# Performance work log

Hardware: AMD Instinct MI355X
Metric: run time of the kernel (lower is better)

Reference implementation:

```python
import jax, jax.numpy as jnp
import numpy as np

ACT_SCALE = 1.0 / 12.0  # nn-EUCLID scale
HIDDEN = 32
BATCH = 1048576


def setup_inputs() -> dict:
    key = jax.random.key(0)
    ks = jax.random.split(key, 12)
    H = HIDDEN

    def xavier(k, shape):
        fan_out, fan_in = shape
        std = (2.0 / (fan_in + fan_out)) ** 0.5
        return jax.random.normal(k, shape, jnp.float32) * std

    def bias(k, fan_in, n):
        bound = 1.0 / (fan_in ** 0.5)
        return jax.random.uniform(k, (n,), jnp.float32, -bound, bound)

    return {
        "eps_flat": jax.random.normal(ks[0], (BATCH, 3), jnp.float32) * 0.1,
        "Bf_w": xavier(ks[1], (H, 2)),
        "Bf_b": bias(ks[2], 2, H),
        "A1": jax.random.normal(ks[3], (H, H), jnp.float32) * 0.05,
        "B1_w": xavier(ks[4], (H, 2)),
        "B1_b": bias(ks[5], 2, H),
        "A2": jax.random.normal(ks[6], (H, H), jnp.float32) * 0.05,
        "B2_w": xavier(ks[7], (H, 2)),
        "B2_b": bias(ks[8], 2, H),
        "A_out": jax.random.normal(ks[9], (1, H), jnp.float32) * 0.05,
        "Bo_w": xavier(ks[10], (1, 2)),
        "Bo_b": bias(ks[11], 2, 1),
    }


def reference(eps_flat, Bf_w, Bf_b, A1, B1_w, B1_b, A2, B2_w, B2_b, A_out, Bo_w, Bo_b):
    sp = jax.nn.softplus

    def W_fn(z0):  # z0: (n, 2) -> (n, 1); ICNN potential (dropout p=0 -> identity)
        z = sp(z0 @ Bf_w.T + Bf_b)
        z = ACT_SCALE * sp(z @ sp(A1).T) ** 2 + sp(z0 @ B1_w.T + B1_b)
        z = ACT_SCALE * sp(z @ sp(A2).T) ** 2 + sp(z0 @ B2_w.T + B2_b)
        return z @ sp(A_out).T + z0 @ Bo_w.T + Bo_b

    e11 = eps_flat[:, 0]
    e22 = eps_flat[:, 1]
    e12 = eps_flat[:, 2]
    I1 = e11 + e22
    I2 = e11 ** 2 + 2.0 * e12 ** 2 + e22 ** 2
    z0 = jnp.stack([I1, I2], axis=-1)  # (B, 2)

    # Reference-point gradient at z0_ref = 0 (makes W(0)=0, dW(0)=0 after correction)
    z0_ref = jnp.zeros((1, 2), eps_flat.dtype)
    grad_ref = jax.grad(lambda z: W_fn(z).sum())(z0_ref)  # (1, 2)

    # Per-sample gradient of corrected potential (rows independent -> grad of sum)
    grads = jax.grad(
        lambda z: (W_fn(z) - (z * grad_ref).sum(-1, keepdims=True)).sum()
    )(z0)  # (B, 2)

    dW_dI1 = grads[:, 0]
    dW_dI2 = grads[:, 1]
    sg = jax.lax.stop_gradient
    s11 = dW_dI1 + 2.0 * sg(e11) * dW_dI2
    s22 = dW_dI1 + 2.0 * sg(e22) * dW_dI2
    s12 = 2.0 * sg(e12) * dW_dI2
    return jnp.stack([s11, s22, s12], axis=-1)
```

## Files before the change

### kernel.cpp

```cpp
#include <hip/hip_runtime.h>
#include <hip/hip_fp16.h>
#include <math.h>

#define ACT_SCALE_F (1.0f / 12.0f)
#define LOG2E_F 1.44269504088896340736f
#define LN2_F   0.69314718055994530942f

typedef __attribute__((ext_vector_type(8))) _Float16 half8;
typedef __attribute__((ext_vector_type(4))) float f32x4;
typedef __attribute__((ext_vector_type(4))) unsigned int uint4v;


__device__ __forceinline__ void sp_sig(float x, float& sp, float& sig) {
    float t = __builtin_amdgcn_exp2f(-fabsf(x) * LOG2E_F);
    float u = 1.0f + t;
    float r = __builtin_amdgcn_rcpf(u);
    sp = fmaf(__builtin_amdgcn_logf(u), LN2_F, fmaxf(x, 0.0f));
    sig = (x >= 0.0f) ? r : t * r;
}

__device__ __forceinline__ float sp_only(float x) {
    float t = __builtin_amdgcn_exp2f(-fabsf(x) * LOG2E_F);
    return fmaf(__builtin_amdgcn_logf(1.0f + t), LN2_F, fmaxf(x, 0.0f));
}

__device__ __forceinline__ float sig_only(float x) {
    float t = __builtin_amdgcn_exp2f(-fabsf(x) * LOG2E_F);
    float r = __builtin_amdgcn_rcpf(1.0f + t);
    return (x >= 0.0f) ? r : t * r;
}

__global__ void prep_kernel(const float* __restrict__ Bf_w, const float* __restrict__ Bf_b,
                            const float* __restrict__ A1,
                            const float* __restrict__ B1_w, const float* __restrict__ B1_b,
                            const float* __restrict__ A2,
                            const float* __restrict__ B2_w, const float* __restrict__ B2_b,
                            const float* __restrict__ A_out,
                            float* __restrict__ ws)
{
    __shared__ float sA1[1024], sA2[1024], sAout[32];
    __shared__ float vbufA[32], vbufB[32];
    __shared__ float part0[32], part1[32];
    const int tid = threadIdx.x;

    for (int e = tid; e < 1024; e += 64) {
        sA1[e] = sp_only(A1[e]);
        sA2[e] = sp_only(A2[e]);
    }
    if (tid < 32) {
        float ao = sp_only(A_out[tid]);
        sAout[tid] = ao;
        ws[384 + tid] = ao;
    }
    __syncthreads();

    unsigned int* wsu = (unsigned int*)ws;
    for (int e = tid; e < 512; e += 64) {
        const int mv = e >> 7, u = (e >> 6) & 1, ln = e & 63;
        const int g = ln >> 4, cc = ln & 15, m = 16 * u + cc;
        for (int q = 0; q < 4; ++q) {
            unsigned int word = 0;
            for (int h = 0; h < 2; ++h) {
                const int s8 = 2 * q + h;
                const int k = 16 * (s8 >> 2) + 4 * g + (s8 & 3);
                float v;
                if (mv == 0)      v = sA1[m * 32 + k];
                else if (mv == 1) v = sA2[m * 32 + k];
                else if (mv == 2) v = sA2[k * 32 + m];
                else              v = sA1[k * 32 + m];
                unsigned short hb = __half_as_ushort(__float2half(v));
                word |= ((unsigned int)hb) << (16 * h);
            }
            wsu[512 + 4 * e + q] = word;
        }
    }

    for (int e = tid; e < 512; e += 64) {
        const int l = e >> 3, s8 = e & 7;
        const int g = l >> 4;
        const int k = 16 * (s8 >> 2) + 4 * g + (s8 & 3);
        ws[2560 + 4 * e]     = Bf_w[2 * k];
        ws[2560 + 4 * e + 1] = Bf_w[2 * k + 1];
        ws[2560 + 4 * e + 2] = Bf_b[k];
        ws[2560 + 4 * e + 3] = 0.f;
        ws[4608 + 4 * e]     = B1_w[2 * k];
        ws[4608 + 4 * e + 1] = B1_w[2 * k + 1];
        ws[4608 + 4 * e + 2] = B1_b[k];
        ws[4608 + 4 * e + 3] = 0.f;
        ws[6656 + 4 * e]     = B2_w[2 * k];
        ws[6656 + 4 * e + 1] = B2_w[2 * k + 1];
        ws[6656 + 4 * e + 2] = B2_b[k];
        ws[6656 + 4 * e + 3] = sAout[k];
    }

    const int i = tid;
    float su1 = 0.f, g1 = 0.f, sb1 = 0.f;
    if (tid < 32) {
        float h0;
        sp_sig(Bf_b[i], h0, su1);
        vbufA[i] = h0;
    }
    __syncthreads();
    if (tid < 32) {
        float a1 = 0.f;
        for (int j = 0; j < 32; ++j) a1 = fmaf(vbufA[j], sA1[i * 32 + j], a1);
        float s1, sa1; sp_sig(a1, s1, sa1);
        g1 = 2.0f * ACT_SCALE_F * s1 * sa1;
        float spb1; sp_sig(B1_b[i], spb1, sb1);
        vbufB[i] = fmaf(ACT_SCALE_F * s1, s1, spb1);
    }
    __syncthreads();
    if (tid < 32) {
        float a2 = 0.f;
        for (int j = 0; j < 32; ++j) a2 = fmaf(vbufB[j], sA2[i * 32 + j], a2);
        float s2, sa2; sp_sig(a2, s2, sa2);
        float g2 = 2.0f * ACT_SCALE_F * s2 * sa2;
        float sb2 = sig_only(B2_b[i]);
        float ao = sAout[i];
        part0[i] = ao * sb2 * B2_w[i * 2 + 0];
        part1[i] = ao * sb2 * B2_w[i * 2 + 1];
        vbufA[i] = ao * g2;
    }
    __syncthreads();
    if (tid < 32) {
        float dz1 = 0.f;
        for (int ii = 0; ii < 32; ++ii) dz1 = fmaf(vbufA[ii], sA2[ii * 32 + i], dz1);
        part0[i] += dz1 * sb1 * B1_w[i * 2 + 0];
        part1[i] += dz1 * sb1 * B1_w[i * 2 + 1];
        vbufB[i] = dz1 * g1;
    }
    __syncthreads();
    if (tid < 32) {
        float dh0 = 0.f;
        for (int ii = 0; ii < 32; ++ii) dh0 = fmaf(vbufB[ii], sA1[ii * 32 + i], dh0);
        part0[i] += dh0 * su1 * Bf_w[i * 2 + 0];
        part1[i] += dh0 * su1 * Bf_w[i * 2 + 1];
    }
    __syncthreads();
    if (tid == 0) {
        float r0 = 0.f, r1 = 0.f;
        for (int j = 0; j < 32; ++j) { r0 += part0[j]; r1 += part1[j]; }
        ws[448] = r0;
        ws[449] = r1;
    }
}

#define DSEL(ch, s8) ((ch) == 0 ? ((s8) < 4 ? dA0[(s8) & 3] : dA1[(s8) & 3]) \
                                : ((s8) < 4 ? dB0[(s8) & 3] : dB1[(s8) & 3]))

__global__ void __launch_bounds__(64, 2) icnn_main(
    const float* __restrict__ eps,
    const float* __restrict__ ws,
    float* __restrict__ out, int n)
{
    const int lane = threadIdx.x;
    const int c = lane & 15;

    int idx0 = blockIdx.x * 32 + c;
    int idx1 = idx0 + 16;
    if (idx0 >= n) idx0 = n - 1;
    if (idx1 >= n) idx1 = n - 1;

    const uint4v* __restrict__ ft = (const uint4v*)((const unsigned int*)ws + 512);
    const float4* __restrict__ Qf = (const float4*)(ws + 2560) + lane * 8;
    const float4* __restrict__ Q1 = (const float4*)(ws + 4608) + lane * 8;
    const float4* __restrict__ Q2 = (const float4*)(ws + 6656) + lane * 8;
    const float gr0 = ws[448], gr1 = ws[449];

    float e11[2], e22[2], e12[2], I1v[2], I2v[2];
    e11[0] = eps[3 * idx0];  e22[0] = eps[3 * idx0 + 1];  e12[0] = eps[3 * idx0 + 2];
    e11[1] = eps[3 * idx1];  e22[1] = eps[3 * idx1 + 1];  e12[1] = eps[3 * idx1 + 2];
    #pragma unroll
    for (int ch = 0; ch < 2; ++ch) {
        I1v[ch] = e11[ch] + e22[ch];
        I2v[ch] = e11[ch] * e11[ch] + 2.f * e12[ch] * e12[ch] + e22[ch] * e22[ch];
    }

    const f32x4 z4 = {0.f, 0.f, 0.f, 0.f};
    unsigned int bwA[4], bwB[4];
    float g1v[2][8];
    float sufx[2][8], sufy[2][8];
    float sb1x[2][8], sb1y[2][8];
    float gx0[2] = {0.f, 0.f}, gx1[2] = {0.f, 0.f};

    #pragma unroll
    for (int m = 0; m < 4; ++m) {
        float pv[2][2];
        #pragma unroll
        for (int h = 0; h < 2; ++h) {
            const int s8 = 2 * m + h;
            const float4 q = Qf[s8];
            #pragma unroll
            for (int ch = 0; ch < 2; ++ch) {
                float h0, su;
                sp_sig(fmaf(I1v[ch], q.x, fmaf(I2v[ch], q.y, q.z)), h0, su);
                sufx[ch][s8] = su * q.x;
                sufy[ch][s8] = su * q.y;
                pv[ch][h] = h0;
            }
        }
        bwA[m] = __builtin_bit_cast(unsigned int, __floats2half2_rn(pv[0][0], pv[0][1]));
        bwB[m] = __builtin_bit_cast(unsigned int, __floats2half2_rn(pv[1][0], pv[1][1]));
    }
    half8 BA = __builtin_bit_cast(half8, (uint4v){bwA[0], bwA[1], bwA[2], bwA[3]});
    half8 BB = __builtin_bit_cast(half8, (uint4v){bwB[0], bwB[1], bwB[2], bwB[3]});

    {
        half8 A0  = __builtin_bit_cast(half8, ft[0 * 64 + lane]);
        half8 A1t = __builtin_bit_cast(half8, ft[1 * 64 + lane]);
        f32x4 dA0 = __builtin_amdgcn_mfma_f32_16x16x32_f16(A0,  BA, z4, 0, 0, 0);
        f32x4 dA1 = __builtin_amdgcn_mfma_f32_16x16x32_f16(A1t, BA, z4, 0, 0, 0);
        f32x4 dB0 = __builtin_amdgcn_mfma_f32_16x16x32_f16(A0,  BB, z4, 0, 0, 0);
        f32x4 dB1 = __builtin_amdgcn_mfma_f32_16x16x32_f16(A1t, BB, z4, 0, 0, 0);
        #pragma unroll
        for (int m = 0; m < 4; ++m) {
            float pv[2][2];
            #pragma unroll
            for (int h = 0; h < 2; ++h) {
                const int s8 = 2 * m + h;
                const float4 q = Q1[s8];
                #pragma unroll
                for (int ch = 0; ch < 2; ++ch) {
                    float a = DSEL(ch, s8);
                    float s1, sg; sp_sig(a, s1, sg);
                    g1v[ch][s8] = (2.0f * ACT_SCALE_F) * s1 * sg;
                    float spb1, sb1;
                    sp_sig(fmaf(I1v[ch], q.x, fmaf(I2v[ch], q.y, q.z)), spb1, sb1);
                    sb1x[ch][s8] = sb1 * q.x;
                    sb1y[ch][s8] = sb1 * q.y;
                    pv[ch][h] = fmaf(ACT_SCALE_F * s1, s1, spb1);
                }
            }
            bwA[m] = __builtin_bit_cast(unsigned int, __floats2half2_rn(pv[0][0], pv[0][1]));
            bwB[m] = __builtin_bit_cast(unsigned int, __floats2half2_rn(pv[1][0], pv[1][1]));
        }
        BA = __builtin_bit_cast(half8, (uint4v){bwA[0], bwA[1], bwA[2], bwA[3]});
        BB = __builtin_bit_cast(half8, (uint4v){bwB[0], bwB[1], bwB[2], bwB[3]});
    }

    {
        half8 A0  = __builtin_bit_cast(half8, ft[2 * 64 + lane]);
        half8 A1t = __builtin_bit_cast(half8, ft[3 * 64 + lane]);
        f32x4 dA0 = __builtin_amdgcn_mfma_f32_16x16x32_f16(A0,  BA, z4, 0, 0, 0);
        f32x4 dA1 = __builtin_amdgcn_mfma_f32_16x16x32_f16(A1t, BA, z4, 0, 0, 0);
        f32x4 dB0 = __builtin_amdgcn_mfma_f32_16x16x32_f16(A0,  BB, z4, 0, 0, 0);
        f32x4 dB1 = __builtin_amdgcn_mfma_f32_16x16x32_f16(A1t, BB, z4, 0, 0, 0);
        #pragma unroll
        for (int m = 0; m < 4; ++m) {
            float pv[2][2];
            #pragma unroll
            for (int h = 0; h < 2; ++h) {
                const int s8 = 2 * m + h;
                const float4 q = Q2[s8];
                #pragma unroll
                for (int ch = 0; ch < 2; ++ch) {
                    float a = DSEL(ch, s8);
                    float s2, sg; sp_sig(a, s2, sg);
                    float sb2 = sig_only(fmaf(I1v[ch], q.x, fmaf(I2v[ch], q.y, q.z)));
                    float ao = q.w;
                    float t = ao * sb2;
                    gx0[ch] = fmaf(t, q.x, gx0[ch]);
                    gx1[ch] = fmaf(t, q.y, gx1[ch]);
                    pv[ch][h] = ao * (2.0f * ACT_SCALE_F) * s2 * sg;
                }
            }
            bwA[m] = __builtin_bit_cast(unsigned int, __floats2half2_rn(pv[0][0], pv[0][1]));
            bwB[m] = __builtin_bit_cast(unsigned int, __floats2half2_rn(pv[1][0], pv[1][1]));
        }
        BA = __builtin_bit_cast(half8, (uint4v){bwA[0], bwA[1], bwA[2], bwA[3]});
        BB = __builtin_bit_cast(half8, (uint4v){bwB[0], bwB[1], bwB[2], bwB[3]});
    }

    {
        half8 A0  = __builtin_bit_cast(half8, ft[4 * 64 + lane]);
        half8 A1t = __builtin_bit_cast(half8, ft[5 * 64 + lane]);
        f32x4 dA0 = __builtin_amdgcn_mfma_f32_16x16x32_f16(A0,  BA, z4, 0, 0, 0);
        f32x4 dA1 = __builtin_amdgcn_mfma_f32_16x16x32_f16(A1t, BA, z4, 0, 0, 0);
        f32x4 dB0 = __builtin_amdgcn_mfma_f32_16x16x32_f16(A0,  BB, z4, 0, 0, 0);
        f32x4 dB1 = __builtin_amdgcn_mfma_f32_16x16x32_f16(A1t, BB, z4, 0, 0, 0);
        #pragma unroll
        for (int m = 0; m < 4; ++m) {
            float pv[2][2];
            #pragma unroll
            for (int h = 0; h < 2; ++h) {
                const int s8 = 2 * m + h;
                #pragma unroll
                for (int ch = 0; ch < 2; ++ch) {
                    float dz = DSEL(ch, s8);
                    gx0[ch] = fmaf(dz, sb1x[ch][s8], gx0[ch]);
                    gx1[ch] = fmaf(dz, sb1y[ch][s8], gx1[ch]);
                    pv[ch][h] = dz * g1v[ch][s8] * (1.0f / 64.0f);
                }
            }
            bwA[m] = __builtin_bit_cast(unsigned int, __floats2half2_rn(pv[0][0], pv[0][1]));
            bwB[m] = __builtin_bit_cast(unsigned int, __floats2half2_rn(pv[1][0], pv[1][1]));
        }
        BA = __builtin_bit_cast(half8, (uint4v){bwA[0], bwA[1], bwA[2], bwA[3]});
        BB = __builtin_bit_cast(half8, (uint4v){bwB[0], bwB[1], bwB[2], bwB[3]});
    }

    {
        half8 A0  = __builtin_bit_cast(half8, ft[6 * 64 + lane]);
        half8 A1t = __builtin_bit_cast(half8, ft[7 * 64 + lane]);
        f32x4 dA0 = __builtin_amdgcn_mfma_f32_16x16x32_f16(A0,  BA, z4, 0, 0, 0);
        f32x4 dA1 = __builtin_amdgcn_mfma_f32_16x16x32_f16(A1t, BA, z4, 0, 0, 0);
        f32x4 dB0 = __builtin_amdgcn_mfma_f32_16x16x32_f16(A0,  BB, z4, 0, 0, 0);
        f32x4 dB1 = __builtin_amdgcn_mfma_f32_16x16x32_f16(A1t, BB, z4, 0, 0, 0);
        float gf0[2] = {0.f, 0.f}, gf1[2] = {0.f, 0.f};
        #pragma unroll
        for (int s8 = 0; s8 < 8; ++s8) {
            #pragma unroll
            for (int ch = 0; ch < 2; ++ch) {
                float dh = DSEL(ch, s8);
                gf0[ch] = fmaf(dh, sufx[ch][s8], gf0[ch]);
                gf1[ch] = fmaf(dh, sufy[ch][s8], gf1[ch]);
            }
        }
        #pragma unroll
        for (int ch = 0; ch < 2; ++ch) {
            gx0[ch] = fmaf(64.f, gf0[ch], gx0[ch]);
            gx1[ch] = fmaf(64.f, gf1[ch], gx1[ch]);
        }
    }

    #pragma unroll
    for (int ch = 0; ch < 2; ++ch) {
        gx0[ch] += __shfl_xor(gx0[ch], 16);
        gx0[ch] += __shfl_xor(gx0[ch], 32);
        gx1[ch] += __shfl_xor(gx1[ch], 16);
        gx1[ch] += __shfl_xor(gx1[ch], 32);
    }

    if (lane < 16) {
        {
            const float dI1 = gx0[0] - gr0;
            const float dI2 = gx1[0] - gr1;
            out[3 * idx0 + 0] = fmaf(2.f * e11[0], dI2, dI1);
            out[3 * idx0 + 1] = fmaf(2.f * e22[0], dI2, dI1);
            out[3 * idx0 + 2] = 2.f * e12[0] * dI2;
        }
        {
            const float dI1 = gx0[1] - gr0;
            const float dI2 = gx1[1] - gr1;
            out[3 * idx1 + 0] = fmaf(2.f * e11[1], dI2, dI1);
            out[3 * idx1 + 1] = fmaf(2.f * e22[1], dI2, dI1);
            out[3 * idx1 + 2] = 2.f * e12[1] * dI2;
        }
    }
}

extern "C" void kernel_launch(void* const* d_in, const int* in_sizes, int n_in,
                              void* d_out, int out_size, void* d_ws, size_t ws_size,
                              hipStream_t stream)
{
    const float* eps   = (const float*)d_in[0];
    const float* Bf_w  = (const float*)d_in[1];
    const float* Bf_b  = (const float*)d_in[2];
    const float* A1    = (const float*)d_in[3];
    const float* B1_w  = (const float*)d_in[4];
    const float* B1_b  = (const float*)d_in[5];
    const float* A2    = (const float*)d_in[6];
    const float* B2_w  = (const float*)d_in[7];
    const float* B2_b  = (const float*)d_in[8];
    const float* A_out = (const float*)d_in[9];

    float* ws  = (float*)d_ws;
    float* out = (float*)d_out;
    const int n = in_sizes[0] / 3;

    prep_kernel<<<1, 64, 0, stream>>>(Bf_w, Bf_b, A1, B1_w, B1_b, A2, B2_w, B2_b, A_out, ws);
    const int blocks = (n + 31) / 32;
    icnn_main<<<blocks, 64, 0, stream>>>(eps, ws, out, n);
}
```

Before: 126.6 us.

## Process four 16-sample chunks per wave and store raw sigmoids to cut registers

Each 64-thread block now handles 64 samples (four chunks of 16) instead of 32. This doubles the MFMA work per weight-fragment load and halves the grid size. To limit register growth, the kernel keeps the raw sigmoid values (su, sb1) and reloads Q weights in the backward pass, instead of holding precomputed products with q.x/q.y. The risk is higher register pressure under launch_bounds(64,2), which could cause spills, and less occupancy-based latency hiding.

```diff
diff --git a/kernel.cpp b/kernel.cpp
--- a/kernel.cpp
+++ b/kernel.cpp
@@ -145,8 +145,8 @@
     }
 }
 
-#define DSEL(ch, s8) ((ch) == 0 ? ((s8) < 4 ? dA0[(s8) & 3] : dA1[(s8) & 3]) \
-                                : ((s8) < 4 ? dB0[(s8) & 3] : dB1[(s8) & 3]))
+#define NCH 4
+#define DSEL(ch, s8) ((s8) < 4 ? dlo[ch][(s8) & 3] : dhi[ch][(s8) & 3])
 
 __global__ void __launch_bounds__(64, 2) icnn_main(
     const float* __restrict__ eps,
@@ -156,10 +156,12 @@
     const int lane = threadIdx.x;
     const int c = lane & 15;
 
-    int idx0 = blockIdx.x * 32 + c;
-    int idx1 = idx0 + 16;
-    if (idx0 >= n) idx0 = n - 1;
-    if (idx1 >= n) idx1 = n - 1;
+    int idx[NCH];
+    #pragma unroll
+    for (int ch = 0; ch < NCH; ++ch) {
+        int id = blockIdx.x * (16 * NCH) + ch * 16 + c;
+        idx[ch] = (id >= n) ? (n - 1) : id;
+    }
 
     const uint4v* __restrict__ ft = (const uint4v*)((const unsigned int*)ws + 512);
     const float4* __restrict__ Qf = (const float4*)(ws + 2560) + lane * 8;
@@ -167,93 +169,103 @@
     const float4* __restrict__ Q2 = (const float4*)(ws + 6656) + lane * 8;
     const float gr0 = ws[448], gr1 = ws[449];
 
-    float e11[2], e22[2], e12[2], I1v[2], I2v[2];
-    e11[0] = eps[3 * idx0];  e22[0] = eps[3 * idx0 + 1];  e12[0] = eps[3 * idx0 + 2];
-    e11[1] = eps[3 * idx1];  e22[1] = eps[3 * idx1 + 1];  e12[1] = eps[3 * idx1 + 2];
-    #pragma unroll
-    for (int ch = 0; ch < 2; ++ch) {
+    float e11[NCH], e22[NCH], e12[NCH], I1v[NCH], I2v[NCH];
+    #pragma unroll
+    for (int ch = 0; ch < NCH; ++ch) {
+        e11[ch] = eps[3 * idx[ch]];
+        e22[ch] = eps[3 * idx[ch] + 1];
+        e12[ch] = eps[3 * idx[ch] + 2];
         I1v[ch] = e11[ch] + e22[ch];
         I2v[ch] = e11[ch] * e11[ch] + 2.f * e12[ch] * e12[ch] + e22[ch] * e22[ch];
     }
 
     const f32x4 z4 = {0.f, 0.f, 0.f, 0.f};
-    unsigned int bwA[4], bwB[4];
-    float g1v[2][8];
-    float sufx[2][8], sufy[2][8];
-    float sb1x[2][8], sb1y[2][8];
-    float gx0[2] = {0.f, 0.f}, gx1[2] = {0.f, 0.f};
+    unsigned int bw[NCH][4];
+    half8 Bv[NCH];
+    float g1v[NCH][8];
+    float su[NCH][8];
+    float sb1[NCH][8];
+    float gx0[NCH], gx1[NCH];
+    #pragma unroll
+    for (int ch = 0; ch < NCH; ++ch) { gx0[ch] = 0.f; gx1[ch] = 0.f; }
 
     #pragma unroll
     for (int m = 0; m < 4; ++m) {
-        float pv[2][2];
+        float pv[NCH][2];
         #pragma unroll
         for (int h = 0; h < 2; ++h) {
             const int s8 = 2 * m + h;
             const float4 q = Qf[s8];
             #pragma unroll
-            for (int ch = 0; ch < 2; ++ch) {
-                float h0, su;
-                sp_sig(fmaf(I1v[ch], q.x, fmaf(I2v[ch], q.y, q.z)), h0, su);
-                sufx[ch][s8] = su * q.x;
-                sufy[ch][s8] = su * q.y;
+            for (int ch = 0; ch < NCH; ++ch) {
+                float h0, sus;
+                sp_sig(fmaf(I1v[ch], q.x, fmaf(I2v[ch], q.y, q.z)), h0, sus);
+                su[ch][s8] = sus;
                 pv[ch][h] = h0;
             }
         }
-        bwA[m] = __builtin_bit_cast(unsigned int, __floats2half2_rn(pv[0][0], pv[0][1]));
-        bwB[m] = __builtin_bit_cast(unsigned int, __floats2half2_rn(pv[1][0], pv[1][1]));
-    }
-    half8 BA = __builtin_bit_cast(half8, (uint4v){bwA[0], bwA[1], bwA[2], bwA[3]});
-    half8 BB = __builtin_bit_cast(half8, (uint4v){bwB[0], bwB[1], bwB[2], bwB[3]});
+        #pragma unroll
+        for (int ch = 0; ch < NCH; ++ch)
+            bw[ch][m] = __builtin_bit_cast(unsigned int, __floats2half2_rn(pv[ch][0], pv[ch][1]));
+    }
+    #pragma unroll
+    for (int ch = 0; ch < NCH; ++ch)
+        Bv[ch] = __builtin_bit_cast(half8, (uint4v){bw[ch][0], bw[ch][1], bw[ch][2], bw[ch][3]});
 
     {
         half8 A0  = __builtin_bit_cast(half8, ft[0 * 64 + lane]);
         half8 A1t = __builtin_bit_cast(half8, ft[1 * 64 + lane]);
-        f32x4 dA0 = __builtin_amdgcn_mfma_f32_16x16x32_f16(A0,  BA, z4, 0, 0, 0);
-        f32x4 dA1 = __builtin_amdgcn_mfma_f32_16x16x32_f16(A1t, BA, z4, 0, 0, 0);
-        f32x4 dB0 = __builtin_amdgcn_mfma_f32_16x16x32_f16(A0,  BB, z4, 0, 0, 0);
-        f32x4 dB1 = __builtin_amdgcn_mfma_f32_16x16x32_f16(A1t, BB, z4, 0, 0, 0);
+        f32x4 dlo[NCH], dhi[NCH];
+        #pragma unroll
+        for (int ch = 0; ch < NCH; ++ch) {
+            dlo[ch] = __builtin_amdgcn_mfma_f32_16x16x32_f16(A0,  Bv[ch], z4, 0, 0, 0);
+            dhi[ch] = __builtin_amdgcn_mfma_f32_16x16x32_f16(A1t, Bv[ch], z4, 0, 0, 0);
+        }
         #pragma unroll
         for (int m = 0; m < 4; ++m) {
-            float pv[2][2];
+            float pv[NCH][2];
             #pragma unroll
             for (int h = 0; h < 2; ++h) {
                 const int s8 = 2 * m + h;
                 const float4 q = Q1[s8];
                 #pragma unroll
-                for (int ch = 0; ch < 2; ++ch) {
+                for (int ch = 0; ch < NCH; ++ch) {
                     float a = DSEL(ch, s8);
                     float s1, sg; sp_sig(a, s1, sg);
                     g1v[ch][s8] = (2.0f * ACT_SCALE_F) * s1 * sg;
-                    float spb1, sb1;
-                    sp_sig(fmaf(I1v[ch], q.x, fmaf(I2v[ch], q.y, q.z)), spb1, sb1);
-                    sb1x[ch][s8] = sb1 * q.x;
-                    sb1y[ch][s8] = sb1 * q.y;
+                    float spb1, sb1s;
+                    sp_sig(fmaf(I1v[ch], q.x, fmaf(I2v[ch], q.y, q.z)), spb1, sb1s);
+                    sb1[ch][s8] = sb1s;
                     pv[ch][h] = fmaf(ACT_SCALE_F * s1, s1, spb1);
                 }
             }
-            bwA[m] = __builtin_bit_cast(unsigned int, __floats2half2_rn(pv[0][0], pv[0][1]));
-            bwB[m] = __builtin_bit_cast(unsigned int, __floats2half2_rn(pv[1][0], pv[1][1]));
-        }
-        BA = __builtin_bit_cast(half8, (uint4v){bwA[0], bwA[1], bwA[2], bwA[3]});
-        BB = __builtin_bit_cast(half8, (uint4v){bwB[0], bwB[1], bwB[2], bwB[3]});
+            #pragma unroll
+            for (int ch = 0; ch < NCH; ++ch)
+                bw[ch][m] = __builtin_bit_cast(unsigned int, __floats2half2_rn(pv[ch][0], pv[ch][1]));
+        }
+        #pragma unroll
+        for (int ch = 0; ch < NCH; ++ch)
+            Bv[ch] = __builtin_bit_cast(half8, (uint4v){bw[ch][0], bw[ch][1], bw[ch][2], bw[ch][3]});
     }
 
     {
         half8 A0  = __builtin_bit_cast(half8, ft[2 * 64 + lane]);
         half8 A1t = __builtin_bit_cast(half8, ft[3 * 64 + lane]);
-        f32x4 dA0 = __builtin_amdgcn_mfma_f32_16x16x32_f16(A0,  BA, z4, 0, 0, 0);
-        f32x4 dA1 = __builtin_amdgcn_mfma_f32_16x16x32_f16(A1t, BA, z4, 0, 0, 0);
-        f32x4 dB0 = __builtin_amdgcn_mfma_f32_16x16x32_f16(A0,  BB, z4, 0, 0, 0);
-        f32x4 dB1 = __builtin_amdgcn_mfma_f32_16x16x32_f16(A1t, BB, z4, 0, 0, 0);
+        f32x4 dlo[NCH], dhi[NCH];
+        #pragma unroll
+        for (int ch = 0; ch < NCH; ++ch) {
+            dlo[ch] = __builtin_amdgcn_mfma_f32_16x16x32_f16(A0,  Bv[ch], z4, 0, 0, 0);
+            dhi[ch] = __builtin_amdgcn_mfma_f32_16x16x32_f16(A1t, Bv[ch], z4, 0, 0, 0);
+        }
         #pragma unroll
         for (int m = 0; m < 4; ++m) {
-            float pv[2][2];
+            float pv[NCH][2];
             #pragma unroll
             for (int h = 0; h < 2; ++h) {
                 const int s8 = 2 * m + h;
                 const float4 q = Q2[s8];
                 #pragma unroll
-                for (int ch = 0; ch < 2; ++ch) {
+                for (int ch = 0; ch < NCH; ++ch) {
                     float a = DSEL(ch, s8);
                     float s2, sg; sp_sig(a, s2, sg);
                     float sb2 = sig_only(fmaf(I1v[ch], q.x, fmaf(I2v[ch], q.y, q.z)));
@@ -264,67 +276,81 @@
                     pv[ch][h] = ao * (2.0f * ACT_SCALE_F) * s2 * sg;
                 }
             }
-            bwA[m] = __builtin_bit_cast(unsigned int, __floats2half2_rn(pv[0][0], pv[0][1]));
-            bwB[m] = __builtin_bit_cast(unsigned int, __floats2half2_rn(pv[1][0], pv[1][1]));
-        }
-        BA = __builtin_bit_cast(half8, (uint4v){bwA[0], bwA[1], bwA[2], bwA[3]});
-        BB = __builtin_bit_cast(half8, (uint4v){bwB[0], bwB[1], bwB[2], bwB[3]});
+            #pragma unroll
+            for (int ch = 0; ch < NCH; ++ch)
+                bw[ch][m] = __builtin_bit_cast(unsigned int, __floats2half2_rn(pv[ch][0], pv[ch][1]));
+        }
+        #pragma unroll
+        for (int ch = 0; ch < NCH; ++ch)
+            Bv[ch] = __builtin_bit_cast(half8, (uint4v){bw[ch][0], bw[ch][1], bw[ch][2], bw[ch][3]});
     }
 
     {
         half8 A0  = __builtin_bit_cast(half8, ft[4 * 64 + lane]);
         half8 A1t = __builtin_bit_cast(half8, ft[5 * 64 + lane]);
-        f32x4 dA0 = __builtin_amdgcn_mfma_f32_16x16x32_f16(A0,  BA, z4, 0, 0, 0);
-        f32x4 dA1 = __builtin_amdgcn_mfma_f32_16x16x32_f16(A1t, BA, z4, 0, 0, 0);
-        f32x4 dB0 = __builtin_amdgcn_mfma_f32_16x16x32_f16(A0,  BB, z4, 0, 0, 0);
-        f32x4 dB1 = __builtin_amdgcn_mfma_f32_16x16x32_f16(A1t, BB, z4, 0, 0, 0);
+        f32x4 dlo[NCH], dhi[NCH];
+        #pragma unroll
+        for (int ch = 0; ch < NCH; ++ch) {
+            dlo[ch] = __builtin_amdgcn_mfma_f32_16x16x32_f16(A0,  Bv[ch], z4, 0, 0, 0);
+            dhi[ch] = __builtin_amdgcn_mfma_f32_16x16x32_f16(A1t, Bv[ch], z4, 0, 0, 0);
+        }
         #pragma unroll
         for (int m = 0; m < 4; ++m) {
-            float pv[2][2];
+            float pv[NCH][2];
             #pragma unroll
             for (int h = 0; h < 2; ++h) {
                 const int s8 = 2 * m + h;
+                const float4 q = Q1[s8];
                 #pragma unroll
-                for (int ch = 0; ch < 2; ++ch) {
+                for (int ch = 0; ch < NCH; ++ch) {
                     float dz = DSEL(ch, s8);
-                    gx0[ch] = fmaf(dz, sb1x[ch][s8], gx0[ch]);
-                    gx1[ch] = fmaf(dz, sb1y[ch][s8], gx1[ch]);
+                    float t = dz * sb1[ch][s8];
+                    gx0[ch] = fmaf(t, q.x, gx0[ch]);
+                    gx1[ch] = fmaf(t, q.y, gx1[ch]);
                     pv[ch][h] = dz * g1v[ch][s8] * (1.0f / 64.0f);
                 }
             }
-            bwA[m] = __builtin_bit_cast(unsigned int, __floats2half2_rn(pv[0][0], pv[0][1]));
-            bwB[m] = __builtin_bit_cast(unsigned int, __floats2half2_rn(pv[1][0], pv[1][1]));
-        }
-        BA = __builtin_bit_cast(half8, (uint4v){bwA[0], bwA[1], bwA[2], bwA[3]});
-        BB = __builtin_bit_cast(half8, (uint4v){bwB[0], bwB[1], bwB[2], bwB[3]});
+            #pragma unroll
+            for (int ch = 0; ch < NCH; ++ch)
+                bw[ch][m] = __builtin_bit_cast(unsigned int, __floats2half2_rn(pv[ch][0], pv[ch][1]));
+        }
+        #pragma unroll
+        for (int ch = 0; ch < NCH; ++ch)
+            Bv[ch] = __builtin_bit_cast(half8, (uint4v){bw[ch][0], bw[ch][1], bw[ch][2], bw[ch][3]});
     }
 
     {
         half8 A0  = __builtin_bit_cast(half8, ft[6 * 64 + lane]);
         half8 A1t = __builtin_bit_cast(half8, ft[7 * 64 + lane]);
-        f32x4 dA0 = __builtin_amdgcn_mfma_f32_16x16x32_f16(A0,  BA, z4, 0, 0, 0);
-        f32x4 dA1 = __builtin_amdgcn_mfma_f32_16x16x32_f16(A1t, BA, z4, 0, 0, 0);
-        f32x4 dB0 = __builtin_amdgcn_mfma_f32_16x16x32_f16(A0,  BB, z4, 0, 0, 0);
-        f32x4 dB1 = __builtin_amdgcn_mfma_f32_16x16x32_f16(A1t, BB, z4, 0, 0, 0);
-        float gf0[2] = {0.f, 0.f}, gf1[2] = {0.f, 0.f};
+        f32x4 dlo[NCH], dhi[NCH];
+        #pragma unroll
+        for (int ch = 0; ch < NCH; ++ch) {
+            dlo[ch] = __builtin_amdgcn_mfma_f32_16x16x32_f16(A0,  Bv[ch], z4, 0, 0, 0);
+            dhi[ch] = __builtin_amdgcn_mfma_f32_16x16x32_f16(A1t, Bv[ch], z4, 0, 0, 0);
+        }
+        float gf0[NCH], gf1[NCH];
+        #pragma unroll
+        for (int ch = 0; ch < NCH; ++ch) { gf0[ch] = 0.f; gf1[ch] = 0.f; }
         #pragma unroll
         for (int s8 = 0; s8 < 8; ++s8) {
-            #pragma unroll
-            for (int ch = 0; ch < 2; ++ch) {
+            const float4 q = Qf[s8];
+            #pragma unroll
+            for (int ch = 0; ch < NCH; ++ch) {
                 float dh = DSEL(ch, s8);
-                gf0[ch] = fmaf(dh, sufx[ch][s8], gf0[ch]);
-                gf1[ch] = fmaf(dh, sufy[ch][s8], gf1[ch]);
-            }
-        }
-        #pragma unroll
-        for (int ch = 0; ch < 2; ++ch) {
+                float t = dh * su[ch][s8];
+                gf0[ch] = fmaf(t, q.x, gf0[ch]);
+                gf1[ch] = fmaf(t, q.y, gf1[ch]);
+            }
+        }
+        #pragma unroll
+        for (int ch = 0; ch < NCH; ++ch) {
             gx0[ch] = fmaf(64.f, gf0[ch], gx0[ch]);
             gx1[ch] = fmaf(64.f, gf1[ch], gx1[ch]);
         }
     }
 
     #pragma unroll
-    for (int ch = 0; ch < 2; ++ch) {
+    for (int ch = 0; ch < NCH; ++ch) {
         gx0[ch] += __shfl_xor(gx0[ch], 16);
         gx0[ch] += __shfl_xor(gx0[ch], 32);
         gx1[ch] += __shfl_xor(gx1[ch], 16);
@@ -332,19 +358,13 @@
     }
 
     if (lane < 16) {
-        {
-            const float dI1 = gx0[0] - gr0;
-            const float dI2 = gx1[0] - gr1;
-            out[3 * idx0 + 0] = fmaf(2.f * e11[0], dI2, dI1);
-            out[3 * idx0 + 1] = fmaf(2.f * e22[0], dI2, dI1);
-            out[3 * idx0 + 2] = 2.f * e12[0] * dI2;
-        }
-        {
-            const float dI1 = gx0[1] - gr0;
-            const float dI2 = gx1[1] - gr1;
-            out[3 * idx1 + 0] = fmaf(2.f * e11[1], dI2, dI1);
-            out[3 * idx1 + 1] = fmaf(2.f * e22[1], dI2, dI1);
-            out[3 * idx1 + 2] = 2.f * e12[1] * dI2;
+        #pragma unroll
+        for (int ch = 0; ch < NCH; ++ch) {
+            const float dI1 = gx0[ch] - gr0;
+            const float dI2 = gx1[ch] - gr1;
+            out[3 * idx[ch] + 0] = fmaf(2.f * e11[ch], dI2, dI1);
+            out[3 * idx[ch] + 1] = fmaf(2.f * e22[ch], dI2, dI1);
+            out[3 * idx[ch] + 2] = 2.f * e12[ch] * dI2;
         }
     }
 }
@@ -369,6 +389,6 @@
     const int n = in_sizes[0] / 3;
 
     prep_kernel<<<1, 64, 0, stream>>>(Bf_w, Bf_b, A1, B1_w, B1_b, A2, B2_w, B2_b, A_out, ws);
-    const int blocks = (n + 31) / 32;
+    const int blocks = (n + 63) / 64;
     icnn_main<<<blocks, 64, 0, stream>>>(eps, ws, out, n);
 }
```

Measured after the change: 346.5 us. 174% more time.
